# Optimization experiments

Measured on AMD Instinct MI355X. Metric: run time of the kernel, lower is better.

Reference implementation:

```python
import jax, jax.numpy as jnp
import numpy as np

N, E, DIN, DOUT = 30000, 480000, 512, 512


def setup_inputs() -> dict:
    key = jax.random.key(0)
    ks = jax.random.split(key, 20)
    inp = {}
    inp["x"] = jax.random.normal(ks[0], (N, DIN), jnp.float32)
    inp["edge_index"] = jax.random.randint(ks[1], (2, E), 0, N, dtype=jnp.int64)
    inp["edge_weight"] = jax.random.uniform(ks[2], (E,), jnp.float32)
    sc = 1.0 / np.sqrt(DIN)
    sl = 1.0 / np.sqrt(2 * DOUT)
    for i, g in enumerate(["i", "f", "g", "o"]):
        inp[f"Wc_{g}"] = jax.random.normal(ks[3 + 4 * i], (DIN, DOUT), jnp.float32) * sc
        inp[f"bc_{g}"] = jnp.zeros((DOUT,), jnp.float32)
        inp[f"Wl_{g}"] = jax.random.normal(ks[4 + 4 * i], (2 * DOUT, DOUT), jnp.float32) * sl
        inp[f"bl_{g}"] = jnp.zeros((DOUT,), jnp.float32)
    return inp


def _gcn_norm(src, dst, w, n):
    # add self loops with weight 1.0 (improved=False), then symmetric normalization
    loops = jnp.arange(n, dtype=src.dtype)
    src = jnp.concatenate([src, loops])
    dst = jnp.concatenate([dst, loops])
    w = jnp.concatenate([w, jnp.ones((n,), w.dtype)])
    deg = jax.ops.segment_sum(w, dst, num_segments=n)
    dinv = jnp.where(deg > 0, jax.lax.rsqrt(jnp.where(deg > 0, deg, 1.0)), 0.0)
    norm = dinv[src] * w * dinv[dst]
    return src, dst, norm


def reference(x, edge_index, edge_weight,
              Wc_i, bc_i, Wl_i, bl_i,
              Wc_f, bc_f, Wl_f, bl_f,
              Wc_g, bc_g, Wl_g, bl_g,
              Wc_o, bc_o, Wl_o, bl_o):
    n = x.shape[0]
    src, dst, norm = _gcn_norm(edge_index[0], edge_index[1], edge_weight, n)
    H = jnp.zeros((n, DOUT), x.dtype)  # _set_hidden_state default
    C = jnp.zeros((n, DOUT), x.dtype)  # _set_cell_state default

    def conv(Wc, bc):
        xw = x @ Wc                                        # [N, DOUT] dense GEMM
        agg = jax.ops.segment_sum(norm[:, None] * xw[src], dst, num_segments=n)
        return agg + bc

    def gate(Wc, bc, Wl, bl, act):
        z = jnp.concatenate([conv(Wc, bc), H], axis=1)      # [N, 2*DOUT]
        return act(z @ Wl + bl)

    I = gate(Wc_i, bc_i, Wl_i, bl_i, jax.nn.sigmoid)
    F = gate(Wc_f, bc_f, Wl_f, bl_f, jax.nn.sigmoid)
    G = gate(Wc_g, bc_g, Wl_g, bl_g, jnp.tanh)
    O = gate(Wc_o, bc_o, Wl_o, bl_o, jax.nn.sigmoid)
    Cn = F * C + I * G
    Hn = O * jnp.tanh(Cn)
    return O, Hn, Cn
```

## Files before the change

### kernel.cpp

```cpp
#include <hip/hip_runtime.h>
#include <stdint.h>

typedef __bf16 bf16;
typedef __attribute__((ext_vector_type(4))) float f4;
typedef __attribute__((ext_vector_type(4))) float f32x4;
typedef __attribute__((ext_vector_type(8))) __bf16 bf8v;
typedef __attribute__((ext_vector_type(4))) __bf16 bf4v;

#define NN 30000
#define MPAD 30080
#define OUTSTRIDE 15360000
#define SC_B 1875

typedef __attribute__((address_space(3))) unsigned int as3_u32;
typedef __attribute__((address_space(1))) unsigned int as1_u32;

__device__ __forceinline__ void gl_lds16(const void* g, void* l) {
  __builtin_amdgcn_global_load_lds((as1_u32*)g, (as3_u32*)l, 16, 0, 0);
}

__global__ void k_pre(const int* __restrict__ ei, const float* __restrict__ ew,
                      void* __restrict__ degcnt, int E) {
  int e = blockIdx.x * 256 + threadIdx.x;
  if (e < E) {
    int d = ei[E + e];
    atomicAdd((float*)degcnt + 2 * d, ew[e]);
    atomicAdd((int*)degcnt + 2 * d + 1, 1);
  }
}

__global__ void k_bsum(const void* __restrict__ degcnt, int* __restrict__ bsum,
                       float* __restrict__ dinv, int n) {
  __shared__ int sm[256];
  int i = blockIdx.x * 256 + threadIdx.x;
  int cnt = 0;
  if (i < n) {
    int2 p = ((const int2*)degcnt)[i];
    cnt = p.y;
    dinv[i] = rsqrtf(__int_as_float(p.x) + 1.0f);
  }
  sm[threadIdx.x] = cnt;
  __syncthreads();
  for (int st = 128; st > 0; st >>= 1) {
    if (threadIdx.x < st) sm[threadIdx.x] += sm[threadIdx.x + st];
    __syncthreads();
  }
  if (threadIdx.x == 0) bsum[blockIdx.x] = sm[0];
}

__global__ void k_bscan(int* bsum, int nb) {
  __shared__ int buf[128];
  int t = threadIdx.x;
  int v = (t < nb) ? bsum[t] : 0;
  buf[t] = v;
  __syncthreads();
  for (int s = 1; s < 128; s <<= 1) {
    int u = (t >= s) ? buf[t - s] : 0;
    __syncthreads();
    buf[t] += u;
    __syncthreads();
  }
  if (t < nb) bsum[t] = buf[t] - v;
}

__global__ void k_offs(const void* __restrict__ degcnt, const int* __restrict__ bsum,
                       int* __restrict__ offs, int n, int E) {
  __shared__ int buf[256];
  int i = blockIdx.x * 256 + threadIdx.x;
  int v = (i < n) ? ((const int*)degcnt)[2 * i + 1] : 0;
  buf[threadIdx.x] = v;
  __syncthreads();
  for (int s = 1; s < 256; s <<= 1) {
    int u = (threadIdx.x >= s) ? buf[threadIdx.x - s] : 0;
    __syncthreads();
    buf[threadIdx.x] += u;
    __syncthreads();
  }
  if (i < n) offs[i] = bsum[blockIdx.x] + buf[threadIdx.x] - v;
  if (i == 0) offs[n] = E;
}

__global__ void k_xbf(const float* __restrict__ x, bf16* __restrict__ xbf, int n8) {
  int i = blockIdx.x * 256 + threadIdx.x;
  if (i >= n8) return;
  const f4* x4 = (const f4*)x;
  f4 a = x4[2 * i], b = x4[2 * i + 1];
  bf8v o;
#pragma unroll
  for (int j = 0; j < 4; ++j) { o[j] = (bf16)a[j]; o[4 + j] = (bf16)b[j]; }
  ((bf8v*)xbf)[i] = o;
}

__global__ void k_fused(const int* __restrict__ ei, const float* __restrict__ ew,
                        const float* __restrict__ dinv, const int* __restrict__ offs,
                        int* __restrict__ cursor, int2* __restrict__ sn, int E,
                        const float* __restrict__ WcA, const float* __restrict__ WlA,
                        const float* __restrict__ WcB, const float* __restrict__ WlB,
                        const float* __restrict__ WcC, const float* __restrict__ WlC,
                        bf16* __restrict__ Wt,
                        const float* __restrict__ bcA, const float* __restrict__ blA,
                        const float* __restrict__ bcB, const float* __restrict__ blB,
                        const float* __restrict__ bcC, const float* __restrict__ blC,
                        float* __restrict__ bcomb) {
  __shared__ float sWc[64][17];
  __shared__ float sWl[16][64];
  __shared__ float smr[4][64];
  int b = blockIdx.x;
  if (b < SC_B) {
    int e = b * 256 + threadIdx.x;
    if (e >= E) return;
    int s = ei[e], d = ei[E + e];
    int pos = offs[d] + atomicAdd(&cursor[d], 1);
    sn[pos] = make_int2(s, __float_as_int(dinv[s] * ew[e] * dinv[d]));
  } else if (b < SC_B + 192) {
    int bb = b - SC_B;
    int g = bb >> 6, rem = bb & 63;
    const float* Wc; const float* Wl;
    if (g == 0)      { Wc = WcA; Wl = WlA; }
    else if (g == 1) { Wc = WcB; Wl = WlB; }
    else             { Wc = WcC; Wl = WlC; }
    int k0 = (rem & 7) * 64, j0 = (rem >> 3) * 64;
    int t = threadIdx.x, tx = t & 15, ty = t >> 4;
    float acc[4][4] = {};
    for (int c0 = 0; c0 < 512; c0 += 16) {
      { int kk = t >> 2, c4 = (t & 3) * 4;
        f4 v = *(const f4*)(Wc + (size_t)(k0 + kk) * 512 + c0 + c4);
#pragma unroll
        for (int j = 0; j < 4; ++j) sWc[kk][c4 + j] = v[j]; }
      { int cc = t >> 4, j4 = (t & 15) * 4;
        f4 v = *(const f4*)(Wl + (size_t)(c0 + cc) * 512 + j0 + j4);
        *(f4*)&sWl[cc][j4] = v; }
      __syncthreads();
#pragma unroll
      for (int cc = 0; cc < 16; ++cc) {
        float wcv[4], wlv[4];
#pragma unroll
        for (int q = 0; q < 4; ++q) wcv[q] = sWc[tx * 4 + q][cc];
#pragma unroll
        for (int a = 0; a < 4; ++a) wlv[a] = sWl[cc][ty * 4 + a];
#pragma unroll
        for (int a = 0; a < 4; ++a)
#pragma unroll
          for (int q = 0; q < 4; ++q) acc[a][q] += wlv[a] * wcv[q];
      }
      __syncthreads();
    }
#pragma unroll
    for (int a = 0; a < 4; ++a) {
      bf4v o;
#pragma unroll
      for (int q = 0; q < 4; ++q) o[q] = (bf16)acc[a][q];
      *(bf4v*)&Wt[((size_t)g * 512 + j0 + ty * 4 + a) * 512 + k0 + tx * 4] = o;
    }
  } else {
    int bb = b - SC_B - 192;
    int g = bb >> 3, jc = bb & 7;
    const float* bc; const float* bl; const float* Wl;
    if (g == 0)      { bc = bcA; bl = blA; Wl = WlA; }
    else if (g == 1) { bc = bcB; bl = blB; Wl = WlB; }
    else             { bc = bcC; bl = blC; Wl = WlC; }
    int jl = threadIdx.x & 63, part = threadIdx.x >> 6;
    int j = jc * 64 + jl;
    float s = 0.f;
    for (int c = part * 128; c < part * 128 + 128; ++c)
      s += bc[c] * Wl[(size_t)c * 512 + j];
    smr[part][jl] = s;
    __syncthreads();
    if (part == 0)
      bcomb[g * 512 + j] = bl[j] + smr[0][jl] + smr[1][jl] + smr[2][jl] + smr[3][jl];
  }
}

__global__ __launch_bounds__(256) void k_agg(const int* __restrict__ offs, const int2* __restrict__ sn,
                                             const float* __restrict__ dinv, const bf16* __restrict__ xbf,
                                             bf16* __restrict__ ybf) {
  int wv = (blockIdx.x * 256 + threadIdx.x) >> 6;
  int lane = threadIdx.x & 63;
  if (wv >= MPAD) return;
  bf16* yrow = ybf + ((size_t)wv << 9) + lane * 8;
  if (wv >= NN) {
    bf8v z;
#pragma unroll
    for (int j = 0; j < 8; ++j) z[j] = (bf16)0.f;
    *(bf8v*)yrow = z;
    return;
  }
  float acc[8];
  float s0 = dinv[wv]; s0 *= s0;
  bf8v xv0 = *(const bf8v*)(xbf + ((size_t)wv << 9) + lane * 8);
#pragma unroll
  for (int j = 0; j < 8; ++j) acc[j] = s0 * (float)xv0[j];
  int e = offs[wv], end = offs[wv + 1];
  for (; e + 4 <= end; e += 4) {
    int2 p0 = sn[e], p1 = sn[e + 1], p2 = sn[e + 2], p3 = sn[e + 3];
    bf8v v0 = *(const bf8v*)(xbf + ((size_t)p0.x << 9) + lane * 8);
    bf8v v1 = *(const bf8v*)(xbf + ((size_t)p1.x << 9) + lane * 8);
    bf8v v2 = *(const bf8v*)(xbf + ((size_t)p2.x << 9) + lane * 8);
    bf8v v3 = *(const bf8v*)(xbf + ((size_t)p3.x << 9) + lane * 8);
    float n0 = __int_as_float(p0.y), n1 = __int_as_float(p1.y);
    float n2 = __int_as_float(p2.y), n3 = __int_as_float(p3.y);
#pragma unroll
    for (int j = 0; j < 8; ++j)
      acc[j] += n0 * (float)v0[j] + n1 * (float)v1[j] + n2 * (float)v2[j] + n3 * (float)v3[j];
  }
  for (; e < end; ++e) {
    int2 p = sn[e];
    bf8v v = *(const bf8v*)(xbf + ((size_t)p.x << 9) + lane * 8);
    float nn = __int_as_float(p.y);
#pragma unroll
    for (int j = 0; j < 8; ++j) acc[j] += nn * (float)v[j];
  }
  bf8v o;
#pragma unroll
  for (int j = 0; j < 8; ++j) o[j] = (bf16)acc[j];
  *(bf8v*)yrow = o;
}

__global__ __launch_bounds__(256, 3) void k_gemm(const bf16* __restrict__ A, const bf16* __restrict__ Bt,
                                                 const float* __restrict__ bcomb, float* __restrict__ out) {
  __shared__ __align__(16) char lds[40960];
  const int t = threadIdx.x, lane = t & 63, w = t >> 6;
  const int wm = w >> 1, wn = w & 1;
  const int d = blockIdx.x;
  const int s = (d & 7) * 235 + (d >> 3);
  const int m0 = (s >> 3) * 128, n0 = (s & 7) * 64;
  const int l15 = lane & 15, lhi = lane >> 4;
  f32x4 acc[3][4][2] = {};

  const int lq = lane >> 2;
  const int sw = (lane >> 3) & 3;
  const int kcol = 16 * ((lane & 3) ^ sw);
  const int rswz = 16 * (lhi ^ ((l15 >> 1) & 3));

  const char* aS[2];
#pragma unroll
  for (int i = 0; i < 2; ++i) {
    int r = (i * 4 + w) * 16 + lq;
    aS[i] = (const char*)A + ((size_t)(m0 + r) << 10) + kcol;
  }
  const char* bS[3];
#pragma unroll
  for (int i = 0; i < 3; ++i) {
    int bi = i * 4 + w, g = bi >> 2, q = bi & 3;
    int n = q * 16 + lq;
    bS[i] = (const char*)Bt + ((size_t)(g * 512 + n0 + n) << 10) + kcol;
  }
  const int vA = (wm * 64 + l15) * 64 + rswz;
  const int vB = 8192 + (wn * 32 + l15) * 64 + rswz;

  auto stage = [&](int bufoff, int kp) {
#pragma unroll
    for (int i = 0; i < 2; ++i)
      gl_lds16(aS[i] + kp * 64, lds + bufoff + (i * 4 + w) * 1024 + lane * 16);
#pragma unroll
    for (int i = 0; i < 3; ++i)
      gl_lds16(bS[i] + kp * 64, lds + bufoff + 8192 + (i * 4 + w) * 1024 + lane * 16);
  };

  auto compute = [&](int bufoff) {
    bf8v af[4];
#pragma unroll
    for (int mi = 0; mi < 4; ++mi)
      af[mi] = *(const bf8v*)(lds + bufoff + vA + mi * 1024);
#pragma unroll
    for (int g = 0; g < 3; ++g) {
      bf8v b0 = *(const bf8v*)(lds + bufoff + vB + g * 4096);
      bf8v b1 = *(const bf8v*)(lds + bufoff + vB + g * 4096 + 1024);
#pragma unroll
      for (int mi = 0; mi < 4; ++mi) {
        acc[g][mi][0] = __builtin_amdgcn_mfma_f32_16x16x32_bf16(b0, af[mi], acc[g][mi][0], 0, 0, 0);
        acc[g][mi][1] = __builtin_amdgcn_mfma_f32_16x16x32_bf16(b1, af[mi], acc[g][mi][1], 0, 0, 0);
      }
    }
  };

  stage(0, 0);
  stage(20480, 1);
#pragma unroll
  for (int kp = 0; kp < 16; ++kp) {
    if (kp < 15) asm volatile("s_waitcnt vmcnt(5)" ::: "memory");
    else         asm volatile("s_waitcnt vmcnt(0)" ::: "memory");
    __builtin_amdgcn_sched_barrier(0);
    __builtin_amdgcn_s_barrier();
    __builtin_amdgcn_sched_barrier(0);
    compute((kp & 1) * 20480);
    __builtin_amdgcn_sched_barrier(0);
    __builtin_amdgcn_s_barrier();
    __builtin_amdgcn_sched_barrier(0);
    if (kp < 14) stage((kp & 1) * 20480, kp + 2);
  }

#pragma unroll
  for (int ni = 0; ni < 2; ++ni) {
    int nb = n0 + wn * 32 + ni * 16 + lhi * 4;
    f4 bI = *(const f4*)&bcomb[nb];
    f4 bG = *(const f4*)&bcomb[512 + nb];
    f4 bO = *(const f4*)&bcomb[1024 + nb];
#pragma unroll
    for (int mi = 0; mi < 4; ++mi) {
      int row = m0 + wm * 64 + mi * 16 + l15;
      if (row < NN) {
        f4 vO, vH, vC;
#pragma unroll
        for (int r = 0; r < 4; ++r) {
          float zi = acc[0][mi][ni][r] + bI[r];
          float zg = acc[1][mi][ni][r] + bG[r];
          float zo = acc[2][mi][ni][r] + bO[r];
          float I = 1.f / (1.f + __expf(-zi));
          float e2g = __expf(2.f * zg);
          float G = (e2g - 1.f) / (e2g + 1.f);
          float O = 1.f / (1.f + __expf(-zo));
          float Cn = I * G;
          float e2c = __expf(2.f * Cn);
          float tc = (e2c - 1.f) / (e2c + 1.f);
          vO[r] = O; vH[r] = O * tc; vC[r] = Cn;
        }
        size_t base = ((size_t)row << 9) + nb;
        *(f4*)&out[base] = vO;
        *(f4*)&out[OUTSTRIDE + base] = vH;
        *(f4*)&out[2 * OUTSTRIDE + base] = vC;
      }
    }
  }
}

extern "C" void kernel_launch(void* const* d_in, const int* in_sizes, int n_in,
                              void* d_out, int out_size, void* d_ws, size_t ws_size,
                              hipStream_t stream) {
  const float* x   = (const float*)d_in[0];
  const int*   ei  = (const int*)d_in[1];
  const float* ew  = (const float*)d_in[2];
  const float* Wc_i = (const float*)d_in[3];
  const float* bc_i = (const float*)d_in[4];
  const float* Wl_i = (const float*)d_in[5];
  const float* bl_i = (const float*)d_in[6];
  const float* Wc_g = (const float*)d_in[11];
  const float* bc_g = (const float*)d_in[12];
  const float* Wl_g = (const float*)d_in[13];
  const float* bl_g = (const float*)d_in[14];
  const float* Wc_o = (const float*)d_in[15];
  const float* bc_o = (const float*)d_in[16];
  const float* Wl_o = (const float*)d_in[17];
  const float* bl_o = (const float*)d_in[18];

  const int E = in_sizes[2];
  const int n = in_sizes[0] / 512;
  const int NB = (n + 255) / 256;

  char* ws = (char*)d_ws;
  bf16*  ybf   = (bf16*)ws;
  float* dinv  = (float*)(ws + 30801920);
  bf16*  Wt    = (bf16*)(ws + 30924800);
  float* bcomb = (float*)(ws + 32497664);
  int*   bsum  = (int*)(ws + 32503808);
  (void)ws_size;

  char* ob = (char*)d_out;
  float* out    = (float*)d_out;
  bf16*  xbf    = (bf16*)ob;
  int2*  sn     = (int2*)(ob + 30720000);
  void*  degcnt = (void*)(ob + 34560000);
  int*   curs   = (int*)(ob + 34800000);
  int*   offs   = (int*)(ob + 34920000);
  (void)out_size; (void)n_in;

  hipMemsetAsync(degcnt, 0, 360000, stream);
  k_xbf<<<(n * 512 / 8 + 255) / 256, 256, 0, stream>>>(x, xbf, n * 512 / 8);
  k_pre<<<(E + 255) / 256, 256, 0, stream>>>(ei, ew, degcnt, E);
  k_bsum<<<NB, 256, 0, stream>>>(degcnt, bsum, dinv, n);
  k_bscan<<<1, 128, 0, stream>>>(bsum, NB);
  k_offs<<<NB, 256, 0, stream>>>(degcnt, bsum, offs, n, E);
  k_fused<<<SC_B + 192 + 24, 256, 0, stream>>>(ei, ew, dinv, offs, curs, sn, E,
                                               Wc_i, Wl_i, Wc_g, Wl_g, Wc_o, Wl_o, Wt,
                                               bc_i, bl_i, bc_g, bl_g, bc_o, bl_o, bcomb);
  k_agg<<<(MPAD * 64 + 255) / 256, 256, 0, stream>>>(offs, sn, dinv, xbf, ybf);
  k_gemm<<<1880, 256, 0, stream>>>(ybf, Wt, bcomb, out);
}
```

Baseline: 301.1 us.

## Halve GEMM M-tile, prefetch edge indices in aggregation, use nontemporal output stores

The GEMM tile shrinks from 128 to 64 rows. Each block now holds less LDS and fewer accumulators, and launch bounds rise to 4 blocks per CU with twice as many blocks, which should improve occupancy and wave balance. The aggregation kernel software-pipelines its edge-index loads one group of four ahead, so the index fetch overlaps the gathers. Output stores become nontemporal to avoid polluting the cache. The smaller tile reloads the B (weight) tiles more often, so per-row arithmetic intensity drops.

```diff
diff --git a/kernel.cpp b/kernel.cpp
--- a/kernel.cpp
+++ b/kernel.cpp
@@ -191,8 +191,11 @@
 #pragma unroll
   for (int j = 0; j < 8; ++j) acc[j] = s0 * (float)xv0[j];
   int e = offs[wv], end = offs[wv + 1];
-  for (; e + 4 <= end; e += 4) {
-    int2 p0 = sn[e], p1 = sn[e + 1], p2 = sn[e + 2], p3 = sn[e + 3];
+  int2 p0, p1, p2, p3;
+  const bool have = (e + 4 <= end);
+  if (have) { p0 = sn[e]; p1 = sn[e + 1]; p2 = sn[e + 2]; p3 = sn[e + 3]; }
+  for (; e + 8 <= end; e += 4) {
+    int2 q0 = sn[e + 4], q1 = sn[e + 5], q2 = sn[e + 6], q3 = sn[e + 7];
     bf8v v0 = *(const bf8v*)(xbf + ((size_t)p0.x << 9) + lane * 8);
     bf8v v1 = *(const bf8v*)(xbf + ((size_t)p1.x << 9) + lane * 8);
     bf8v v2 = *(const bf8v*)(xbf + ((size_t)p2.x << 9) + lane * 8);
@@ -202,6 +205,19 @@
 #pragma unroll
     for (int j = 0; j < 8; ++j)
       acc[j] += n0 * (float)v0[j] + n1 * (float)v1[j] + n2 * (float)v2[j] + n3 * (float)v3[j];
+    p0 = q0; p1 = q1; p2 = q2; p3 = q3;
+  }
+  if (have) {
+    bf8v v0 = *(const bf8v*)(xbf + ((size_t)p0.x << 9) + lane * 8);
+    bf8v v1 = *(const bf8v*)(xbf + ((size_t)p1.x << 9) + lane * 8);
+    bf8v v2 = *(const bf8v*)(xbf + ((size_t)p2.x << 9) + lane * 8);
+    bf8v v3 = *(const bf8v*)(xbf + ((size_t)p3.x << 9) + lane * 8);
+    float n0 = __int_as_float(p0.y), n1 = __int_as_float(p1.y);
+    float n2 = __int_as_float(p2.y), n3 = __int_as_float(p3.y);
+#pragma unroll
+    for (int j = 0; j < 8; ++j)
+      acc[j] += n0 * (float)v0[j] + n1 * (float)v1[j] + n2 * (float)v2[j] + n3 * (float)v3[j];
+    e += 4;
   }
   for (; e < end; ++e) {
     int2 p = sn[e];
@@ -216,58 +232,50 @@
   *(bf8v*)yrow = o;
 }
 
-__global__ __launch_bounds__(256, 3) void k_gemm(const bf16* __restrict__ A, const bf16* __restrict__ Bt,
+__global__ __launch_bounds__(256, 4) void k_gemm(const bf16* __restrict__ A, const bf16* __restrict__ Bt,
                                                  const float* __restrict__ bcomb, float* __restrict__ out) {
-  __shared__ __align__(16) char lds[40960];
+  __shared__ __align__(16) char lds[32768];
   const int t = threadIdx.x, lane = t & 63, w = t >> 6;
   const int wm = w >> 1, wn = w & 1;
   const int d = blockIdx.x;
-  const int s = (d & 7) * 235 + (d >> 3);
-  const int m0 = (s >> 3) * 128, n0 = (s & 7) * 64;
+  const int s = (d & 7) * 470 + (d >> 3);
+  const int m0 = (s >> 3) * 64, n0 = (s & 7) * 64;
   const int l15 = lane & 15, lhi = lane >> 4;
-  f32x4 acc[3][4][2] = {};
+  f32x4 acc[3][2][2] = {};
 
   const int lq = lane >> 2;
   const int sw = (lane >> 3) & 3;
   const int kcol = 16 * ((lane & 3) ^ sw);
   const int rswz = 16 * (lhi ^ ((l15 >> 1) & 3));
 
-  const char* aS[2];
-#pragma unroll
-  for (int i = 0; i < 2; ++i) {
-    int r = (i * 4 + w) * 16 + lq;
-    aS[i] = (const char*)A + ((size_t)(m0 + r) << 10) + kcol;
-  }
+  const char* aS = (const char*)A + ((size_t)(m0 + w * 16 + lq) << 10) + kcol;
   const char* bS[3];
 #pragma unroll
   for (int i = 0; i < 3; ++i) {
     int bi = i * 4 + w, g = bi >> 2, q = bi & 3;
-    int n = q * 16 + lq;
-    bS[i] = (const char*)Bt + ((size_t)(g * 512 + n0 + n) << 10) + kcol;
-  }
-  const int vA = (wm * 64 + l15) * 64 + rswz;
-  const int vB = 8192 + (wn * 32 + l15) * 64 + rswz;
+    bS[i] = (const char*)Bt + ((size_t)(g * 512 + n0 + q * 16 + lq) << 10) + kcol;
+  }
+  const int vA = (wm * 32 + l15) * 64 + rswz;
+  const int vB = 4096 + (wn * 32 + l15) * 64 + rswz;
 
   auto stage = [&](int bufoff, int kp) {
-#pragma unroll
-    for (int i = 0; i < 2; ++i)
-      gl_lds16(aS[i] + kp * 64, lds + bufoff + (i * 4 + w) * 1024 + lane * 16);
+    gl_lds16(aS + kp * 64, lds + bufoff + w * 1024 + lane * 16);
 #pragma unroll
     for (int i = 0; i < 3; ++i)
-      gl_lds16(bS[i] + kp * 64, lds + bufoff + 8192 + (i * 4 + w) * 1024 + lane * 16);
+      gl_lds16(bS[i] + kp * 64, lds + bufoff + 4096 + (i * 4 + w) * 1024 + lane * 16);
   };
 
   auto compute = [&](int bufoff) {
-    bf8v af[4];
-#pragma unroll
-    for (int mi = 0; mi < 4; ++mi)
+    bf8v af[2];
+#pragma unroll
+    for (int mi = 0; mi < 2; ++mi)
       af[mi] = *(const bf8v*)(lds + bufoff + vA + mi * 1024);
 #pragma unroll
     for (int g = 0; g < 3; ++g) {
       bf8v b0 = *(const bf8v*)(lds + bufoff + vB + g * 4096);
       bf8v b1 = *(const bf8v*)(lds + bufoff + vB + g * 4096 + 1024);
 #pragma unroll
-      for (int mi = 0; mi < 4; ++mi) {
+      for (int mi = 0; mi < 2; ++mi) {
         acc[g][mi][0] = __builtin_amdgcn_mfma_f32_16x16x32_bf16(b0, af[mi], acc[g][mi][0], 0, 0, 0);
         acc[g][mi][1] = __builtin_amdgcn_mfma_f32_16x16x32_bf16(b1, af[mi], acc[g][mi][1], 0, 0, 0);
       }
@@ -275,19 +283,19 @@
   };
 
   stage(0, 0);
-  stage(20480, 1);
+  stage(16384, 1);
 #pragma unroll
   for (int kp = 0; kp < 16; ++kp) {
-    if (kp < 15) asm volatile("s_waitcnt vmcnt(5)" ::: "memory");
+    if (kp < 15) asm volatile("s_waitcnt vmcnt(4)" ::: "memory");
     else         asm volatile("s_waitcnt vmcnt(0)" ::: "memory");
     __builtin_amdgcn_sched_barrier(0);
     __builtin_amdgcn_s_barrier();
     __builtin_amdgcn_sched_barrier(0);
-    compute((kp & 1) * 20480);
+    compute((kp & 1) * 16384);
     __builtin_amdgcn_sched_barrier(0);
     __builtin_amdgcn_s_barrier();
     __builtin_amdgcn_sched_barrier(0);
-    if (kp < 14) stage((kp & 1) * 20480, kp + 2);
+    if (kp < 14) stage((kp & 1) * 16384, kp + 2);
   }
 
 #pragma unroll
@@ -297,8 +305,8 @@
     f4 bG = *(const f4*)&bcomb[512 + nb];
     f4 bO = *(const f4*)&bcomb[1024 + nb];
 #pragma unroll
-    for (int mi = 0; mi < 4; ++mi) {
-      int row = m0 + wm * 64 + mi * 16 + l15;
+    for (int mi = 0; mi < 2; ++mi) {
+      int row = m0 + wm * 32 + mi * 16 + l15;
       if (row < NN) {
         f4 vO, vH, vC;
 #pragma unroll
@@ -316,9 +324,9 @@
           vO[r] = O; vH[r] = O * tc; vC[r] = Cn;
         }
         size_t base = ((size_t)row << 9) + nb;
-        *(f4*)&out[base] = vO;
-        *(f4*)&out[OUTSTRIDE + base] = vH;
-        *(f4*)&out[2 * OUTSTRIDE + base] = vC;
+        __builtin_nontemporal_store(vO, (f4*)&out[base]);
+        __builtin_nontemporal_store(vH, (f4*)&out[OUTSTRIDE + base]);
+        __builtin_nontemporal_store(vC, (f4*)&out[2 * OUTSTRIDE + base]);
       }
     }
   }
@@ -374,5 +382,5 @@
                                                Wc_i, Wl_i, Wc_g, Wl_g, Wc_o, Wl_o, Wt,
                                                bc_i, bl_i, bc_g, bl_g, bc_o, bl_o, bcomb);
   k_agg<<<(MPAD * 64 + 255) / 256, 256, 0, stream>>>(offs, sn, dinv, xbf, ybf);
-  k_gemm<<<1880, 256, 0, stream>>>(ybf, Wt, bcomb, out);
-}
+  k_gemm<<<3760, 256, 0, stream>>>(ybf, Wt, bcomb, out);
+}
```

Measured after the change: 303.8 us. No clear change (+0.9%).
